# Performance work log

Measured on AMD Instinct MI355X. Metric: run time of the kernel, lower is better.

The kernel has to match this reference:

```python
import jax, jax.numpy as jnp
import numpy as np

BS, P, R, D = 32, 128, 16, 1024
RHO = 0.97
EPS = 1e-8


def unit_normalize(x):
    return x / jnp.maximum(jnp.linalg.norm(x, axis=-1, keepdims=True), EPS)


def setup_inputs() -> dict:
    key = jax.random.key(0)
    ks = jax.random.split(key, 12)
    scale = 1.0 / np.sqrt(D)
    return {
        "x_all": jax.random.normal(ks[0], (BS, P, D), jnp.float32),
        "h_all": jax.random.normal(ks[1], (BS, P, D), jnp.float32),
        "surprise_all": jax.random.uniform(ks[2], (BS, P, 1), jnp.float32) * 8.0,
        "reset_mask": jax.random.bernoulli(ks[3], 0.05, (BS, P)),
        "pm_K": unit_normalize(jax.random.normal(ks[4], (BS, R, D), jnp.float32)),
        "pm_V": unit_normalize(jax.random.normal(ks[5], (BS, R, D), jnp.float32)),
        "pm_a": jax.random.uniform(ks[6], (BS, R), jnp.float32),
        "elig_K0": jnp.zeros((BS, R, D), jnp.float32),
        "elig_V0": jnp.zeros((BS, R, D), jnp.float32),
        "W_k": jax.random.normal(ks[7], (D, D), jnp.float32) * scale,
        "b_k": jnp.zeros((D,), jnp.float32),
        "W_v": jax.random.normal(ks[8], (D, D), jnp.float32) * scale,
        "b_v": jnp.zeros((D,), jnp.float32),
    }


def reference(x_all, h_all, surprise_all, reset_mask, pm_K, pm_V, pm_a,
              elig_K0, elig_V0, W_k, b_k, W_v, b_v):
    # ---- apply_batch: read-only slot-memory readout over P tokens ----
    x_q = unit_normalize(x_all)                                  # [BS,P,D]
    scores = jnp.einsum('brd,bpd->bpr', pm_K, x_q)               # [BS,P,R]
    weighted = pm_a[:, None, :] * scores                         # [BS,P,R]
    y_pm = jnp.einsum('bpr,brd->bpd', weighted, pm_V)            # [BS,P,D]

    # ---- update_eligibility_batch: affine scan over P tokens ----
    k_cand = unit_normalize(jnp.einsum('bpd,de->bpe', x_all, W_k) + b_k)  # [BS,P,D]
    v_cand = jnp.einsum('bpd,de->bpe', h_all, W_v) + b_v                  # [BS,P,D]
    gate = jnp.clip(surprise_all[..., 0] / 5.0, 0.0, 1.0)                 # [BS,P]
    a_keep = RHO * (1.0 - reset_mask.astype(jnp.float32))                 # [BS,P]

    def step(carry, inp):
        eK, eV = carry                      # each [BS,R,D]
        k, v, g, a = inp                    # [BS,D],[BS,D],[BS],[BS]
        # b_t = gate * cand, broadcast across the R slots (matches torch expand)
        eK = a[:, None, None] * eK + (g[:, None] * k)[:, None, :]
        eV = a[:, None, None] * eV + (g[:, None] * v)[:, None, :]
        return (eK, eV), None

    xs = (jnp.swapaxes(k_cand, 0, 1), jnp.swapaxes(v_cand, 0, 1),
          gate.T, a_keep.T)                 # leading axis = P
    (elig_K, elig_V), _ = jax.lax.scan(step, (elig_K0, elig_V0), xs)

    return y_pm, elig_K, elig_V
```

## Files before the change

### kernel.cpp

```cpp
#include <hip/hip_runtime.h>
#include <cstdint>
#include <cstddef>

#define NB 32
#define NP 128
#define NR 16
#define ND 1024
#define RHOC 0.97f
#define EPSN 1e-8f

typedef short bf16x8 __attribute__((ext_vector_type(8)));
typedef float f32x4 __attribute__((ext_vector_type(4)));
typedef unsigned short u16x8 __attribute__((ext_vector_type(8)));
typedef unsigned short ushort_t;

__device__ inline ushort_t f2bf(float f) {
  unsigned u = __float_as_uint(f);
  unsigned r = (u + 0x7fffu + ((u >> 16) & 1u)) >> 16;
  return (ushort_t)r;
}
__device__ inline float bf2f(ushort_t v) {
  return __uint_as_float(((unsigned)v) << 16);
}
__device__ inline void gload16(const void* g, void* l) {
  __builtin_amdgcn_global_load_lds(
      (const __attribute__((address_space(1))) void*)g,
      (__attribute__((address_space(3))) void*)l, 16, 0, 0);
}

__global__ __launch_bounds__(256) void prep_kernel(
    const float* __restrict__ surprise, const void* __restrict__ mask,
    const float* __restrict__ x, const float* __restrict__ Wk,
    const float* __restrict__ pmK,
    float* __restrict__ c, float* __restrict__ Abuf, float* __restrict__ csum,
    ushort_t* __restrict__ Xb, float* __restrict__ xnorm,
    ushort_t* __restrict__ WkT, ushort_t* __restrict__ pmKb) {
  __shared__ __align__(16) char smem[8448];
  int bid = blockIdx.x;
  int t = threadIdx.x;
  if (bid < NB) {
    float* a_sh = (float*)smem;
    float* suf  = a_sh + 128;
    float* redc = suf + 132;
    int*   isu8 = (int*)(redc + 128);
    int b = bid;
    if (t == 0) *isu8 = 0;
    __syncthreads();
    const unsigned char* mb = (const unsigned char*)mask;
    int v = 0;
    for (int i = t; i < NB * NP; i += 256)
      if ((i & 3) != 0 && mb[i] != 0) v = 1;
    if (v) *isu8 = 1;
    __syncthreads();
    int u8 = *isu8;
    if (t < NP) {
      int mv = u8 ? mb[b * NP + t] : ((const int*)mask)[b * NP + t];
      a_sh[t] = RHOC * (mv ? 0.f : 1.f);
    }
    __syncthreads();
    if (t == 0) {
      float p = 1.f;
      suf[NP] = 1.f;
      for (int s = NP - 1; s >= 0; --s) { p *= a_sh[s]; suf[s] = p; }
    }
    __syncthreads();
    if (t < NP) {
      float g = fminf(fmaxf(surprise[b * NP + t] * 0.2f, 0.f), 1.f);
      float cv = g * suf[t + 1];
      c[b * NP + t] = cv;
      redc[t] = cv;
    }
    __syncthreads();
    for (int off = 64; off > 0; off >>= 1) {
      if (t < off) redc[t] += redc[t + off];
      __syncthreads();
    }
    if (t == 0) { csum[b] = redc[0]; Abuf[b] = suf[0]; }
  } else if (bid < NB + NB * NP) {
    int row = bid - NB;
    float* red = (float*)smem;
    float4 vv = *(const float4*)&x[(size_t)row * ND + t * 4];
    ushort4 o;
    o.x = f2bf(vv.x); o.y = f2bf(vv.y); o.z = f2bf(vv.z); o.w = f2bf(vv.w);
    *(ushort4*)&Xb[(size_t)row * ND + t * 4] = o;
    float ss = vv.x * vv.x + vv.y * vv.y + vv.z * vv.z + vv.w * vv.w;
#pragma unroll
    for (int off = 32; off > 0; off >>= 1) ss += __shfl_xor(ss, off);
    int wave = t >> 6, lane = t & 63;
    if (lane == 0) red[wave] = ss;
    __syncthreads();
    if (t == 0) xnorm[row] = sqrtf(red[0] + red[1] + red[2] + red[3]);
  } else if (bid < NB + NB * NP + 256) {
    int id2 = bid - (NB + NB * NP);
    ushort_t (*tt)[65] = (ushort_t(*)[65])smem;
    int k0 = (id2 >> 4) * 64, n0 = (id2 & 15) * 64;
#pragma unroll
    for (int i = 0; i < 16; ++i) {
      int r = i * 4 + (t >> 6), cc = t & 63;
      tt[r][cc] = f2bf(Wk[(size_t)(k0 + r) * ND + n0 + cc]);
    }
    __syncthreads();
#pragma unroll
    for (int i = 0; i < 16; ++i) {
      int r = i * 4 + (t >> 6), cc = t & 63;
      WkT[(size_t)(n0 + r) * ND + k0 + cc] = tt[cc][r];
    }
  } else {
    int id3 = bid - (NB + NB * NP + 256);
    size_t base = (size_t)id3 * 2048 + t * 8;
    float4 a = *(const float4*)&pmK[base];
    float4 bq = *(const float4*)&pmK[base + 4];
    u16x8 o;
    o[0] = f2bf(a.x); o[1] = f2bf(a.y); o[2] = f2bf(a.z); o[3] = f2bf(a.w);
    o[4] = f2bf(bq.x); o[5] = f2bf(bq.y); o[6] = f2bf(bq.z); o[7] = f2bf(bq.w);
    *(u16x8*)&pmKb[base] = o;
  }
}

__global__ __launch_bounds__(256) void main_kernel(
    const ushort_t* __restrict__ Xb, const ushort_t* __restrict__ WkT,
    const float* __restrict__ bk, float* __restrict__ norms2p,
    const float* __restrict__ h, const float* __restrict__ c,
    float* __restrict__ hbar,
    const ushort_t* __restrict__ pmKb, const float* __restrict__ pmV,
    const float* __restrict__ pma, const float* __restrict__ xnorm,
    float* __restrict__ y) {
  __shared__ __align__(16) char smem[25600];
  int bid = blockIdx.x;
  int tid = threadIdx.x;
  if (bid < 512) {
    ushort_t* As = (ushort_t*)smem;
    ushort_t* Bs = As + 128 * 64;
    float* sred = (float*)(Bs + 64 * 64);
    int lane = tid & 63, wid = tid >> 6;
    int wr = wid >> 1, wc = wid & 1;
    int bm = bid & 31, bn = bid >> 5;
    int m0 = bm * 128, n0 = bn * 64;
    int lo = lane & 15, hi = lane >> 4;
    f32x4 acc[4][2] = {};
    for (int k0 = 0; k0 < ND; k0 += 64) {
#pragma unroll
      for (int i = 0; i < 4; ++i) {
        int sl = i * 256 + tid;
        int r = sl >> 3, s = sl & 7;
        int gk = k0 + ((s ^ (r & 7)) << 3);
        gload16(&Xb[(size_t)(m0 + r) * ND + gk], &As[sl << 3]);
      }
#pragma unroll
      for (int i = 0; i < 2; ++i) {
        int sl = i * 256 + tid;
        int r = sl >> 3, s = sl & 7;
        int gk = k0 + ((s ^ (r & 7)) << 3);
        gload16(&WkT[(size_t)(n0 + r) * ND + gk], &Bs[sl << 3]);
      }
      __syncthreads();
#pragma unroll
      for (int ksl = 0; ksl < 2; ++ksl) {
        bf16x8 af[4], bfr[2];
#pragma unroll
        for (int mi = 0; mi < 4; ++mi) {
          int r = wr * 64 + mi * 16 + lo;
          int s = (ksl * 4 + hi) ^ (r & 7);
          af[mi] = *(const bf16x8*)&As[(r << 6) + (s << 3)];
        }
#pragma unroll
        for (int ni = 0; ni < 2; ++ni) {
          int r = wc * 32 + ni * 16 + lo;
          int s = (ksl * 4 + hi) ^ (r & 7);
          bfr[ni] = *(const bf16x8*)&Bs[(r << 6) + (s << 3)];
        }
#pragma unroll
        for (int mi = 0; mi < 4; ++mi)
#pragma unroll
          for (int ni = 0; ni < 2; ++ni)
            acc[mi][ni] = __builtin_amdgcn_mfma_f32_16x16x32_bf16(
                af[mi], bfr[ni], acc[mi][ni], 0, 0, 0);
      }
      __syncthreads();
    }
    float bkv[2];
#pragma unroll
    for (int ni = 0; ni < 2; ++ni) bkv[ni] = bk[n0 + wc * 32 + ni * 16 + lo];
#pragma unroll
    for (int mi = 0; mi < 4; ++mi) {
#pragma unroll
      for (int j = 0; j < 4; ++j) {
        float ss = 0.f;
#pragma unroll
        for (int ni = 0; ni < 2; ++ni) {
          float vv = acc[mi][ni][j] + bkv[ni];
          ss += vv * vv;
        }
        ss += __shfl_xor(ss, 1);
        ss += __shfl_xor(ss, 2);
        ss += __shfl_xor(ss, 4);
        ss += __shfl_xor(ss, 8);
        if (lo == 0) sred[wc * 128 + wr * 64 + mi * 16 + hi * 4 + j] = ss;
      }
    }
    __syncthreads();
    if (tid < 128)
      norms2p[(size_t)bn * (NB * NP) + m0 + tid] = sred[tid] + sred[128 + tid];
  } else if (bid < 1024) {
    int id = bid - 512;
    int b = id >> 4, dchunk = id & 15;
    float* cs = (float*)smem;
    float* red = cs + 128;
    int dd = tid & 63, sl = tid >> 6;
    int d = dchunk * 64 + dd;
    if (tid < NP) cs[tid] = c[b * NP + tid];
    __syncthreads();
    const float* hb = h + ((size_t)b * NP + sl * 32) * ND + d;
    float acc = 0.f;
#pragma unroll
    for (int tt2 = 0; tt2 < 32; ++tt2) acc += cs[sl * 32 + tt2] * hb[(size_t)tt2 * ND];
    red[sl * 64 + dd] = acc;
    __syncthreads();
    if (sl == 0)
      hbar[(size_t)b * ND + d] = red[dd] + red[64 + dd] + red[128 + dd] + red[192 + dd];
  } else {
    int id2 = bid - 1024;
    int b = id2 >> 3, p0 = (id2 & 7) * 16;
    float* sredp = (float*)smem;
    float* wls = sredp + 4 * 16 * 17;
    int lane = tid & 63, wid = tid >> 6;
    int lo = lane & 15, hi = lane >> 4;
    float4 v[16];
#pragma unroll
    for (int r = 0; r < 16; ++r)
      v[r] = *(const float4*)&pmV[((size_t)(b * NR + r)) * ND + tid * 4];
    const ushort_t* xrow = &Xb[((size_t)(b * NP + p0 + lo)) * ND];
    const ushort_t* krow = &pmKb[((size_t)(b * NR + lo)) * ND];
    f32x4 sc = {};
#pragma unroll
    for (int ki = 0; ki < 8; ++ki) {
      int koff = (wid * 8 + ki) * 32 + hi * 8;
      bf16x8 af = *(const bf16x8*)&xrow[koff];
      bf16x8 bf = *(const bf16x8*)&krow[koff];
      sc = __builtin_amdgcn_mfma_f32_16x16x32_bf16(af, bf, sc, 0, 0, 0);
    }
#pragma unroll
    for (int j = 0; j < 4; ++j) sredp[(wid * 16 + hi * 4 + j) * 17 + lo] = sc[j];
    __syncthreads();
    {
      int p = tid >> 4, r = tid & 15;
      float s = sredp[(p)*17 + r] + sredp[(16 + p) * 17 + r] +
                sredp[(32 + p) * 17 + r] + sredp[(48 + p) * 17 + r];
      wls[p * 16 + r] = pma[b * NR + r] * s / fmaxf(xnorm[b * NP + p0 + p], EPSN);
    }
    __syncthreads();
#pragma unroll
    for (int p = 0; p < 16; ++p) {
      float4 a = {0.f, 0.f, 0.f, 0.f};
#pragma unroll
      for (int r = 0; r < 16; ++r) {
        float w = wls[p * 16 + r];
        a.x += w * v[r].x; a.y += w * v[r].y;
        a.z += w * v[r].z; a.w += w * v[r].w;
      }
      *(float4*)&y[((size_t)(b * NP + p0 + p)) * ND + tid * 4] = a;
    }
  }
}

__device__ __forceinline__ void vkbar_body(
    int id2, int t, int path, const float* __restrict__ src,
    const float* __restrict__ W, float* __restrict__ partials, char* smemv) {
  float (*hst)[36] = (float(*)[36])smemv;
  int esl = id2 >> 4, dchunk = id2 & 15;
  int e0 = esl * 128, d0 = dchunk * 64;
#pragma unroll
  for (int i = 0; i < 16; ++i) {
    int idx = i * 256 + t;
    int bb = idx >> 7, e = idx & 127;
    hst[e][bb] = src[(size_t)bb * ND + e0 + e];
  }
  __syncthreads();
  int bg = t >> 6, dd = t & 63, d = d0 + dd;
  float acc[8] = {};
  for (int e = 0; e < 128; ++e) {
    float w = W[(size_t)(e0 + e) * ND + d];
    float4 h0 = *(const float4*)&hst[e][bg * 8];
    float4 h1 = *(const float4*)&hst[e][bg * 8 + 4];
    acc[0] += h0.x * w; acc[1] += h0.y * w; acc[2] += h0.z * w; acc[3] += h0.w * w;
    acc[4] += h1.x * w; acc[5] += h1.y * w; acc[6] += h1.z * w; acc[7] += h1.w * w;
  }
#pragma unroll
  for (int i = 0; i < 8; ++i)
    partials[((size_t)(path * 8 + esl) * NB + bg * 8 + i) * ND + d] = acc[i];
}

__device__ __forceinline__ void epi_body(
    int id2, int t, int path, const float* __restrict__ partials,
    const float* __restrict__ bias, const float* __restrict__ coef,
    const float* __restrict__ e0p, const float* __restrict__ Abuf,
    float* __restrict__ out) {
  int b = id2 >> 2, dc = id2 & 3;
  int d = dc * 256 + t;
  float s = 0.f;
#pragma unroll
  for (int sl = 0; sl < 8; ++sl)
    s += partials[((size_t)(path * 8 + sl) * NB + b) * ND + d];
  s += coef[b] * bias[d];
  float A = Abuf[b];
#pragma unroll
  for (int r = 0; r < NR; ++r) {
    size_t idx = ((size_t)(b * NR + r)) * ND + d;
    out[idx] = A * e0p[idx] + s;
  }
}

__global__ __launch_bounds__(256) void d3_kernel(
    const ushort_t* __restrict__ Xb, const float* __restrict__ norms2p,
    const float* __restrict__ c, float* __restrict__ xbar,
    float* __restrict__ wsum,
    const float* __restrict__ hbar, const float* __restrict__ Wv,
    float* __restrict__ partials) {
  __shared__ __align__(16) char smem[18432];
  int bid = blockIdx.x;
  int tid = threadIdx.x;
  if (bid < 256) {
    float* wsh = (float*)smem;
    float* red = wsh + NP;
    int b = bid >> 3;
    int dd = tid & 63, sl = tid >> 6;
    int d = (bid & 7) * 128 + dd * 2;
    if (tid < NP) {
      float s = 0.f;
#pragma unroll
      for (int pc = 0; pc < 16; ++pc)
        s += norms2p[(size_t)pc * (NB * NP) + b * NP + tid];
      wsh[tid] = c[b * NP + tid] / fmaxf(sqrtf(s), EPSN);
    }
    __syncthreads();
    if ((bid & 7) == 0 && tid == 0) {
      float s = 0.f;
      for (int t2 = 0; t2 < NP; ++t2) s += wsh[t2];
      wsum[b] = s;
    }
    const ushort_t* xb = Xb + ((size_t)b * NP + sl * 32) * ND + d;
    float ax = 0.f, ay = 0.f;
#pragma unroll
    for (int t2 = 0; t2 < 32; ++t2) {
      unsigned u = *(const unsigned*)&xb[(size_t)t2 * ND];
      float w = wsh[sl * 32 + t2];
      ax += w * bf2f((ushort_t)(u & 0xffffu));
      ay += w * bf2f((ushort_t)(u >> 16));
    }
    red[(sl * 64 + dd) * 2 + 0] = ax;
    red[(sl * 64 + dd) * 2 + 1] = ay;
    __syncthreads();
    if (sl == 0) {
      float2 o;
      o.x = red[dd * 2] + red[(64 + dd) * 2] + red[(128 + dd) * 2] + red[(192 + dd) * 2];
      o.y = red[dd * 2 + 1] + red[(64 + dd) * 2 + 1] + red[(128 + dd) * 2 + 1] +
            red[(192 + dd) * 2 + 1];
      *(float2*)&xbar[(size_t)b * ND + d] = o;
    }
  } else {
    vkbar_body(bid - 256, tid, 0, hbar, Wv, partials, smem);
  }
}

__global__ __launch_bounds__(256) void d4_kernel(
    const float* __restrict__ xbar, const float* __restrict__ Wk,
    float* __restrict__ partials,
    const float* __restrict__ bv, const float* __restrict__ csum,
    const float* __restrict__ eV0, const float* __restrict__ Abuf,
    float* __restrict__ outV) {
  __shared__ __align__(16) char smem[18432];
  int bid = blockIdx.x;
  int tid = threadIdx.x;
  if (bid < 128) {
    vkbar_body(bid, tid, 1, xbar, Wk, partials, smem);
  } else {
    epi_body(bid - 128, tid, 0, partials, bv, csum, eV0, Abuf, outV);
  }
}

__global__ __launch_bounds__(256) void d5_kernel(
    const float* __restrict__ partials, const float* __restrict__ bk,
    const float* __restrict__ wsum, const float* __restrict__ eK0,
    const float* __restrict__ Abuf, float* __restrict__ outK) {
  epi_body(blockIdx.x, threadIdx.x, 1, partials, bk, wsum, eK0, Abuf, outK);
}

extern "C" void kernel_launch(void* const* d_in, const int* in_sizes, int n_in,
                              void* d_out, int out_size, void* d_ws, size_t ws_size,
                              hipStream_t stream) {
  (void)in_sizes; (void)n_in; (void)out_size; (void)ws_size;
  const float* x_all    = (const float*)d_in[0];
  const float* h_all    = (const float*)d_in[1];
  const float* surprise = (const float*)d_in[2];
  const void*  mask     = d_in[3];
  const float* pmK      = (const float*)d_in[4];
  const float* pmV      = (const float*)d_in[5];
  const float* pma      = (const float*)d_in[6];
  const float* eK0      = (const float*)d_in[7];
  const float* eV0      = (const float*)d_in[8];
  const float* Wk       = (const float*)d_in[9];
  const float* bk       = (const float*)d_in[10];
  const float* Wv       = (const float*)d_in[11];
  const float* bv       = (const float*)d_in[12];

  float* y    = (float*)d_out;
  float* outK = y + (size_t)NB * NP * ND;
  float* outV = outK + (size_t)NB * NR * ND;

  char* w = (char*)d_ws;
  float* c        = (float*)w; w += NB * NP * 4;
  float* Abuf     = (float*)w; w += 256;
  float* csum     = (float*)w; w += 256;
  float* wsum     = (float*)w; w += 256;
  float* hbar     = (float*)w; w += NB * ND * 4;
  float* xbar     = (float*)w; w += NB * ND * 4;
  float* norms2p  = (float*)w; w += (size_t)16 * NB * NP * 4;
  float* xnorm    = (float*)w; w += NB * NP * 4;
  float* partials = (float*)w; w += (size_t)16 * NB * ND * 4;
  ushort_t* WkT   = (ushort_t*)w; w += (size_t)ND * ND * 2;
  ushort_t* pmKb  = (ushort_t*)w; w += (size_t)NB * NR * ND * 2;
  ushort_t* Xb    = (ushort_t*)w; w += (size_t)NB * NP * ND * 2;

  prep_kernel<<<NB + NB * NP + 256 + 256, 256, 0, stream>>>(
      surprise, mask, x_all, Wk, pmK, c, Abuf, csum, Xb, xnorm, WkT, pmKb);
  main_kernel<<<512 + 512 + 256, 256, 0, stream>>>(
      Xb, WkT, bk, norms2p, h_all, c, hbar, pmKb, pmV, pma, xnorm, y);
  d3_kernel<<<256 + 128, 256, 0, stream>>>(Xb, norms2p, c, xbar, wsum, hbar,
                                           Wv, partials);
  d4_kernel<<<128 + 128, 256, 0, stream>>>(xbar, Wk, partials, bv, csum, eV0,
                                           Abuf, outV);
  d5_kernel<<<128, 256, 0, stream>>>(partials, bk, wsum, eK0, Abuf, outK);
}
```

Baseline: 60.31 us.

## Move slot-memory readout into prep kernel reading fp32 x and pmK directly

The y readout blocks move from main_kernel into prep_kernel. They now load fp32 x and pm_K directly, convert them in registers with v_cvt_pk_bf16_f32, and compute the row norms of x inline. This drops the pmKb conversion blocks, the xnorm buffer and the per-row norm reduction, and shortens main_kernel. The X to bf16 conversion also switches to the hardware packed-convert instruction. In exchange the readout rereads fp32 x at twice the bytes, and it now runs alongside prep work instead of the GEMM.

```diff
diff --git a/kernel.cpp b/kernel.cpp
--- a/kernel.cpp
+++ b/kernel.cpp
@@ -11,7 +11,6 @@
 
 typedef short bf16x8 __attribute__((ext_vector_type(8)));
 typedef float f32x4 __attribute__((ext_vector_type(4)));
-typedef unsigned short u16x8 __attribute__((ext_vector_type(8)));
 typedef unsigned short ushort_t;
 
 __device__ inline ushort_t f2bf(float f) {
@@ -22,6 +21,14 @@
 __device__ inline float bf2f(ushort_t v) {
   return __uint_as_float(((unsigned)v) << 16);
 }
+__device__ inline bf16x8 cvt8(float4 a, float4 b) {
+  union { bf16x8 v; unsigned u[4]; } o;
+  asm("v_cvt_pk_bf16_f32 %0, %1, %2" : "=v"(o.u[0]) : "v"(a.x), "v"(a.y));
+  asm("v_cvt_pk_bf16_f32 %0, %1, %2" : "=v"(o.u[1]) : "v"(a.z), "v"(a.w));
+  asm("v_cvt_pk_bf16_f32 %0, %1, %2" : "=v"(o.u[2]) : "v"(b.x), "v"(b.y));
+  asm("v_cvt_pk_bf16_f32 %0, %1, %2" : "=v"(o.u[3]) : "v"(b.z), "v"(b.w));
+  return o.v;
+}
 __device__ inline void gload16(const void* g, void* l) {
   __builtin_amdgcn_global_load_lds(
       (const __attribute__((address_space(1))) void*)g,
@@ -31,19 +38,72 @@
 __global__ __launch_bounds__(256) void prep_kernel(
     const float* __restrict__ surprise, const void* __restrict__ mask,
     const float* __restrict__ x, const float* __restrict__ Wk,
-    const float* __restrict__ pmK,
+    const float* __restrict__ pmK, const float* __restrict__ pmV,
+    const float* __restrict__ pma,
     float* __restrict__ c, float* __restrict__ Abuf, float* __restrict__ csum,
-    ushort_t* __restrict__ Xb, float* __restrict__ xnorm,
-    ushort_t* __restrict__ WkT, ushort_t* __restrict__ pmKb) {
+    ushort_t* __restrict__ Xb, ushort_t* __restrict__ WkT,
+    float* __restrict__ y) {
   __shared__ __align__(16) char smem[8448];
   int bid = blockIdx.x;
   int t = threadIdx.x;
-  if (bid < NB) {
+  if (bid < 256) {
+    int b = bid >> 3, p0 = (bid & 7) * 16;
+    float* sredp = (float*)smem;
+    float* wls = sredp + 4 * 16 * 17;
+    float* rowssq = wls + 256;
+    int lane = t & 63, wid = t >> 6;
+    int lo = lane & 15, hi = lane >> 4;
+    float4 v[16];
+#pragma unroll
+    for (int r = 0; r < 16; ++r)
+      v[r] = *(const float4*)&pmV[((size_t)(b * NR + r)) * ND + t * 4];
+    const float* xrow = &x[((size_t)(b * NP + p0 + lo)) * ND];
+    const float* krow = &pmK[((size_t)(b * NR + lo)) * ND];
+    f32x4 sc = {};
+    float ssq = 0.f;
+#pragma unroll
+    for (int ki = 0; ki < 8; ++ki) {
+      int koff = (wid * 8 + ki) * 32 + hi * 8;
+      float4 xa = *(const float4*)&xrow[koff];
+      float4 xc = *(const float4*)&xrow[koff + 4];
+      ssq += xa.x * xa.x + xa.y * xa.y + xa.z * xa.z + xa.w * xa.w +
+             xc.x * xc.x + xc.y * xc.y + xc.z * xc.z + xc.w * xc.w;
+      float4 ka = *(const float4*)&krow[koff];
+      float4 kc = *(const float4*)&krow[koff + 4];
+      sc = __builtin_amdgcn_mfma_f32_16x16x32_bf16(cvt8(xa, xc), cvt8(ka, kc),
+                                                   sc, 0, 0, 0);
+    }
+    ssq += __shfl_xor(ssq, 16);
+    ssq += __shfl_xor(ssq, 32);
+    if (hi == 0) rowssq[wid * 16 + lo] = ssq;
+#pragma unroll
+    for (int j = 0; j < 4; ++j) sredp[(wid * 16 + hi * 4 + j) * 17 + lo] = sc[j];
+    __syncthreads();
+    {
+      int p = t >> 4, r = t & 15;
+      float s = sredp[p * 17 + r] + sredp[(16 + p) * 17 + r] +
+                sredp[(32 + p) * 17 + r] + sredp[(48 + p) * 17 + r];
+      float nrm = sqrtf(rowssq[p] + rowssq[16 + p] + rowssq[32 + p] + rowssq[48 + p]);
+      wls[p * 16 + r] = pma[b * NR + r] * s / fmaxf(nrm, EPSN);
+    }
+    __syncthreads();
+#pragma unroll
+    for (int p = 0; p < 16; ++p) {
+      float4 a = {0.f, 0.f, 0.f, 0.f};
+#pragma unroll
+      for (int r = 0; r < 16; ++r) {
+        float w = wls[p * 16 + r];
+        a.x += w * v[r].x; a.y += w * v[r].y;
+        a.z += w * v[r].z; a.w += w * v[r].w;
+      }
+      *(float4*)&y[((size_t)(b * NP + p0 + p)) * ND + t * 4] = a;
+    }
+  } else if (bid < 256 + NB) {
+    int b = bid - 256;
     float* a_sh = (float*)smem;
     float* suf  = a_sh + 128;
     float* redc = suf + 132;
     int*   isu8 = (int*)(redc + 128);
-    int b = bid;
     if (t == 0) *isu8 = 0;
     __syncthreads();
     const unsigned char* mb = (const unsigned char*)mask;
@@ -76,22 +136,15 @@
       __syncthreads();
     }
     if (t == 0) { csum[b] = redc[0]; Abuf[b] = suf[0]; }
-  } else if (bid < NB + NB * NP) {
-    int row = bid - NB;
-    float* red = (float*)smem;
+  } else if (bid < 256 + NB + NB * NP) {
+    int row = bid - (256 + NB);
     float4 vv = *(const float4*)&x[(size_t)row * ND + t * 4];
-    ushort4 o;
-    o.x = f2bf(vv.x); o.y = f2bf(vv.y); o.z = f2bf(vv.z); o.w = f2bf(vv.w);
-    *(ushort4*)&Xb[(size_t)row * ND + t * 4] = o;
-    float ss = vv.x * vv.x + vv.y * vv.y + vv.z * vv.z + vv.w * vv.w;
-#pragma unroll
-    for (int off = 32; off > 0; off >>= 1) ss += __shfl_xor(ss, off);
-    int wave = t >> 6, lane = t & 63;
-    if (lane == 0) red[wave] = ss;
-    __syncthreads();
-    if (t == 0) xnorm[row] = sqrtf(red[0] + red[1] + red[2] + red[3]);
-  } else if (bid < NB + NB * NP + 256) {
-    int id2 = bid - (NB + NB * NP);
+    union { unsigned u[2]; ushort4 s4; } o;
+    asm("v_cvt_pk_bf16_f32 %0, %1, %2" : "=v"(o.u[0]) : "v"(vv.x), "v"(vv.y));
+    asm("v_cvt_pk_bf16_f32 %0, %1, %2" : "=v"(o.u[1]) : "v"(vv.z), "v"(vv.w));
+    *(ushort4*)&Xb[(size_t)row * ND + t * 4] = o.s4;
+  } else {
+    int id2 = bid - (256 + NB + NB * NP);
     ushort_t (*tt)[65] = (ushort_t(*)[65])smem;
     int k0 = (id2 >> 4) * 64, n0 = (id2 & 15) * 64;
 #pragma unroll
@@ -105,15 +158,6 @@
       int r = i * 4 + (t >> 6), cc = t & 63;
       WkT[(size_t)(n0 + r) * ND + k0 + cc] = tt[cc][r];
     }
-  } else {
-    int id3 = bid - (NB + NB * NP + 256);
-    size_t base = (size_t)id3 * 2048 + t * 8;
-    float4 a = *(const float4*)&pmK[base];
-    float4 bq = *(const float4*)&pmK[base + 4];
-    u16x8 o;
-    o[0] = f2bf(a.x); o[1] = f2bf(a.y); o[2] = f2bf(a.z); o[3] = f2bf(a.w);
-    o[4] = f2bf(bq.x); o[5] = f2bf(bq.y); o[6] = f2bf(bq.z); o[7] = f2bf(bq.w);
-    *(u16x8*)&pmKb[base] = o;
   }
 }
 
@@ -121,10 +165,7 @@
     const ushort_t* __restrict__ Xb, const ushort_t* __restrict__ WkT,
     const float* __restrict__ bk, float* __restrict__ norms2p,
     const float* __restrict__ h, const float* __restrict__ c,
-    float* __restrict__ hbar,
-    const ushort_t* __restrict__ pmKb, const float* __restrict__ pmV,
-    const float* __restrict__ pma, const float* __restrict__ xnorm,
-    float* __restrict__ y) {
+    float* __restrict__ hbar) {
   __shared__ __align__(16) char smem[25600];
   int bid = blockIdx.x;
   int tid = threadIdx.x;
@@ -201,7 +242,7 @@
     __syncthreads();
     if (tid < 128)
       norms2p[(size_t)bn * (NB * NP) + m0 + tid] = sred[tid] + sred[128 + tid];
-  } else if (bid < 1024) {
+  } else {
     int id = bid - 512;
     int b = id >> 4, dchunk = id & 15;
     float* cs = (float*)smem;
@@ -218,48 +259,6 @@
     __syncthreads();
     if (sl == 0)
       hbar[(size_t)b * ND + d] = red[dd] + red[64 + dd] + red[128 + dd] + red[192 + dd];
-  } else {
-    int id2 = bid - 1024;
-    int b = id2 >> 3, p0 = (id2 & 7) * 16;
-    float* sredp = (float*)smem;
-    float* wls = sredp + 4 * 16 * 17;
-    int lane = tid & 63, wid = tid >> 6;
-    int lo = lane & 15, hi = lane >> 4;
-    float4 v[16];
-#pragma unroll
-    for (int r = 0; r < 16; ++r)
-      v[r] = *(const float4*)&pmV[((size_t)(b * NR + r)) * ND + tid * 4];
-    const ushort_t* xrow = &Xb[((size_t)(b * NP + p0 + lo)) * ND];
-    const ushort_t* krow = &pmKb[((size_t)(b * NR + lo)) * ND];
-    f32x4 sc = {};
-#pragma unroll
-    for (int ki = 0; ki < 8; ++ki) {
-      int koff = (wid * 8 + ki) * 32 + hi * 8;
-      bf16x8 af = *(const bf16x8*)&xrow[koff];
-      bf16x8 bf = *(const bf16x8*)&krow[koff];
-      sc = __builtin_amdgcn_mfma_f32_16x16x32_bf16(af, bf, sc, 0, 0, 0);
-    }
-#pragma unroll
-    for (int j = 0; j < 4; ++j) sredp[(wid * 16 + hi * 4 + j) * 17 + lo] = sc[j];
-    __syncthreads();
-    {
-      int p = tid >> 4, r = tid & 15;
-      float s = sredp[(p)*17 + r] + sredp[(16 + p) * 17 + r] +
-                sredp[(32 + p) * 17 + r] + sredp[(48 + p) * 17 + r];
-      wls[p * 16 + r] = pma[b * NR + r] * s / fmaxf(xnorm[b * NP + p0 + p], EPSN);
-    }
-    __syncthreads();
-#pragma unroll
-    for (int p = 0; p < 16; ++p) {
-      float4 a = {0.f, 0.f, 0.f, 0.f};
-#pragma unroll
-      for (int r = 0; r < 16; ++r) {
-        float w = wls[p * 16 + r];
-        a.x += w * v[r].x; a.y += w * v[r].y;
-        a.z += w * v[r].z; a.w += w * v[r].w;
-      }
-      *(float4*)&y[((size_t)(b * NP + p0 + p)) * ND + tid * 4] = a;
-    }
   }
 }
 
@@ -415,16 +414,13 @@
   float* hbar     = (float*)w; w += NB * ND * 4;
   float* xbar     = (float*)w; w += NB * ND * 4;
   float* norms2p  = (float*)w; w += (size_t)16 * NB * NP * 4;
-  float* xnorm    = (float*)w; w += NB * NP * 4;
   float* partials = (float*)w; w += (size_t)16 * NB * ND * 4;
   ushort_t* WkT   = (ushort_t*)w; w += (size_t)ND * ND * 2;
-  ushort_t* pmKb  = (ushort_t*)w; w += (size_t)NB * NR * ND * 2;
   ushort_t* Xb    = (ushort_t*)w; w += (size_t)NB * NP * ND * 2;
 
-  prep_kernel<<<NB + NB * NP + 256 + 256, 256, 0, stream>>>(
-      surprise, mask, x_all, Wk, pmK, c, Abuf, csum, Xb, xnorm, WkT, pmKb);
-  main_kernel<<<512 + 512 + 256, 256, 0, stream>>>(
-      Xb, WkT, bk, norms2p, h_all, c, hbar, pmKb, pmV, pma, xnorm, y);
+  prep_kernel<<<256 + NB + NB * NP + 256, 256, 0, stream>>>(
+      surprise, mask, x_all, Wk, pmK, pmV, pma, c, Abuf, csum, Xb, WkT, y);
+  main_kernel<<<512 + 512, 256, 0, stream>>>(Xb, WkT, bk, norms2p, h_all, c, hbar);
   d3_kernel<<<256 + 128, 256, 0, stream>>>(Xb, norms2p, c, xbar, wsum, hbar,
                                            Wv, partials);
   d4_kernel<<<128 + 128, 256, 0, stream>>>(xbar, Wk, partials, bv, csum, eV0,
```

Result: slower. 62.16 us (+3.1%).
